# Kernel optimization log

Measured on AMD Instinct MI355X. Metric: run time of the kernel, lower is better.

## Reference

```python
import jax, jax.numpy as jnp
import numpy as np

N = 100_000      # nodes
E = 1_600_000    # directed edges (before self-loops)
F_IN = 256       # input node features
H = 128          # hidden_dim
HEADS = 2
C_HEAD = H // HEADS  # 64, GATConv out_channels per head
G = 128          # graphs in batch
NCLS = 10
NEG_SLOPE = 0.2  # PyG GATConv default


def setup_inputs() -> dict:
    key = jax.random.key(0)
    ks = jax.random.split(key, 20)
    p = lambda k, shape: (jax.random.normal(k, shape, jnp.float32) * 0.05)
    x = jax.random.normal(ks[0], (N, F_IN), jnp.float32)
    edge_index = jax.random.randint(ks[1], (2, E), 0, N, dtype=jnp.int64)
    batch = jnp.sort(jax.random.randint(ks[2], (N,), 0, G, dtype=jnp.int64))
    return dict(
        x=x, edge_index=edge_index, batch=batch,
        pre_w=p(ks[3], (F_IN, H)), pre_b=p(ks[4], (H,)),
        w1=p(ks[5], (H, H)), asrc1=p(ks[6], (HEADS, C_HEAD)), adst1=p(ks[7], (HEADS, C_HEAD)), b1=p(ks[8], (H,)),
        w2=p(ks[9], (H, H)), asrc2=p(ks[10], (HEADS, C_HEAD)), adst2=p(ks[11], (HEADS, C_HEAD)), b2=p(ks[12], (H,)),
        post_w1=p(ks[13], (H, H)), post_b1=p(ks[14], (H,)),
        post_w2=p(ks[15], (H, NCLS)), post_b2=p(ks[16], (NCLS,)),
    )


def _gat_conv(h_in, w, a_src, a_dst, b, src, dst):
    # h: [N, heads, c]
    h = (h_in @ w).reshape(N, HEADS, C_HEAD)
    alpha_src = jnp.sum(h * a_src, axis=-1)  # [N, heads]
    alpha_dst = jnp.sum(h * a_dst, axis=-1)  # [N, heads]
    e = jax.nn.leaky_relu(alpha_src[src] + alpha_dst[dst], NEG_SLOPE)  # [E+N, heads]
    # numerically stable softmax over incoming edges of each destination node
    m = jax.ops.segment_max(e, dst, num_segments=N)
    ex = jnp.exp(e - m[dst])
    denom = jax.ops.segment_sum(ex, dst, num_segments=N)
    alpha = ex / denom[dst]                                           # [E+N, heads]
    out = jax.ops.segment_sum(h[src] * alpha[:, :, None], dst, num_segments=N)
    return out.reshape(N, H) + b  # concat heads + bias


def reference(x, edge_index, batch, pre_w, pre_b,
              w1, asrc1, adst1, b1, w2, asrc2, adst2, b2,
              post_w1, post_b1, post_w2, post_b2):
    # PyG GATConv default add_self_loops=True
    loop = jnp.arange(N, dtype=edge_index.dtype)
    src = jnp.concatenate([edge_index[0], loop])
    dst = jnp.concatenate([edge_index[1], loop])

    h = jax.nn.relu(x @ pre_w + pre_b)
    reprs = jax.ops.segment_sum(h, batch, num_segments=G)
    h = jax.nn.relu(_gat_conv(h, w1, asrc1, adst1, b1, src, dst))
    reprs = reprs + jax.ops.segment_sum(h, batch, num_segments=G)
    h = jax.nn.relu(_gat_conv(h, w2, asrc2, adst2, b2, src, dst))
    reprs = reprs + jax.ops.segment_sum(h, batch, num_segments=G)
    z = jax.nn.relu(reprs @ post_w1 + post_b1) @ post_w2 + post_b2
    return jax.nn.log_softmax(z, axis=-1)
```

## Files before the change

### kernel.cpp

```cpp
#include <hip/hip_runtime.h>
#include <hip/hip_bf16.h>
#include <math.h>

#define NNODES 100000
#define NEDGES 1600000
#define FIN 256
#define HDIM 128
#define NGRAPH 128
#define NCLS 10
#define NEG 0.2f

#define NBUCK 98
#define EPB 4096
#define EBLK ((NEDGES + EPB - 1) / EPB)

typedef short bf8 __attribute__((ext_vector_type(8)));
typedef float f4 __attribute__((ext_vector_type(4)));
typedef float f2v __attribute__((ext_vector_type(2)));

__device__ __forceinline__ float lrelu(float x) { return x > 0.f ? x : NEG * x; }

__device__ __forceinline__ unsigned short f2bf(float f) {
  union { float f; unsigned int u; } v; v.f = f;
  unsigned int r = v.u + 0x7fffu + ((v.u >> 16) & 1u);
  return (unsigned short)(r >> 16);
}
__device__ __forceinline__ float bf2f(unsigned short u) {
  union { unsigned int u; float f; } v; v.u = ((unsigned int)u) << 16; return v.f;
}
__device__ __forceinline__ float fast_rcp(float x) {
  float r;
  asm("v_rcp_f32 %0, %1" : "=v"(r) : "v"(x));
  return r;
}
__device__ __forceinline__ unsigned cvt_pk_bf16(float lo, float hi) {
  unsigned r;
  asm("v_cvt_pk_bf16_f32 %0, %1, %2" : "=v"(r) : "v"(lo), "v"(hi));
  return r;
}
__device__ __forceinline__ unsigned short pk_fp8(float a, float b) {
  return (unsigned short)__builtin_amdgcn_cvt_pk_fp8_f32(a, b, 0, false);
}
__device__ __forceinline__ f2v pk_unpack_fp8(unsigned p) {
#if __has_builtin(__builtin_amdgcn_cvt_pk_f32_fp8)
  return __builtin_amdgcn_cvt_pk_f32_fp8((int)p, false);
#else
  f2v r;
  r.x = __builtin_amdgcn_cvt_f32_fp8(p, 0);
  r.y = __builtin_amdgcn_cvt_f32_fp8(p, 1);
  return r;
#endif
}

__global__ __launch_bounds__(256) void convert_transpose(const float* __restrict__ w,
                                                         unsigned short* __restrict__ wt,
                                                         int K) {
  int i = blockIdx.x * 256 + threadIdx.x;
  if (i >= K * 128) return;
  int k = i >> 7, n = i & 127;
  wt[n * K + k] = f2bf(w[(size_t)k * 128 + n]);
}

template<int K, int ABF16>
__global__ __launch_bounds__(256) void gemm_cstage(const void* __restrict__ Av,
                                                   const unsigned short* __restrict__ Bt,
                                                   const float* __restrict__ bias,
                                                   unsigned short* __restrict__ Cb,
                                                   unsigned short* __restrict__ Cp,
                                                   const float* __restrict__ a_src,
                                                   const float* __restrict__ a_dst,
                                                   float* __restrict__ o_as,
                                                   float* __restrict__ o_ad,
                                                   int M, int dorelu) {
  constexpr int NKT = K / 32;
  __shared__ alignas(16) char AL[NKT * 256 * 16];
  __shared__ alignas(16) char BL[4 * 512 * 16];
  int tid = threadIdx.x;
  int wv = tid >> 6, lane = tid & 63;
  int quad = lane >> 4, m16 = lane & 15;
  int row0 = blockIdx.x * 64;

  if (ABF16) {
    const unsigned short* A = (const unsigned short*)Av;
    constexpr int UPR = K / 8;
#pragma unroll
    for (int i = 0; i < (64 * UPR) / 256; ++i) {
      int m = i * 256 + tid;
      int row = m / UPR;
      int u = m & (UPR - 1);
      int rr = row0 + row; if (rr > M - 1) rr = M - 1;
      bf8 v = *(const bf8*)&A[(size_t)rr * K + u * 8];
      int kt = u >> 2, q = u & 3;
      int dst = (((kt * 256) + (row >> 4) * 64 + q * 16 + (row & 15)) * 16) ^ ((kt & 7) << 4);
      *(bf8*)(AL + dst) = v;
    }
  } else {
    const float* A = (const float*)Av;
    constexpr int UPRF = K / 4;
#pragma unroll
    for (int i = 0; i < (64 * UPRF) / 256; ++i) {
      int m = i * 256 + tid;
      int row = m / UPRF;
      int u = m & (UPRF - 1);
      int rr = row0 + row; if (rr > M - 1) rr = M - 1;
      float4 v = *(const float4*)&A[(size_t)rr * K + u * 4];
      int kt = u >> 3, q = (u >> 1) & 3;
      int dst = ((kt * 256 + (row >> 4) * 64 + q * 16 + (row & 15)) * 16 + (u & 1) * 8) ^ ((kt & 7) << 4);
      uint2 w; w.x = cvt_pk_bf16(v.x, v.y); w.y = cvt_pk_bf16(v.z, v.w);
      *(uint2*)(AL + dst) = w;
    }
  }

  auto stageB = [&](int ch) {
#pragma unroll
    for (int i = 0; i < 8; ++i) {
      int m = i * 256 + tid;
      int nrow = m >> 4;
      int u = m & 15;
      bf8 v = *(const bf8*)&Bt[(size_t)nrow * K + ch * 128 + u * 8];
      int ktl = u >> 2;
      int dst = ((ktl * 512 + (nrow >> 4) * 64 + (u & 3) * 16 + (nrow & 15)) * 16) ^ (ktl << 4);
      *(bf8*)(BL + dst) = v;
    }
  };

  f4 acc[8];
#pragma unroll
  for (int b = 0; b < 8; ++b) acc[b] = (f4){0.f, 0.f, 0.f, 0.f};

  stageB(0);
  __syncthreads();
  constexpr int NCH = K / 128;
#pragma unroll
  for (int ch = 0; ch < NCH; ++ch) {
    if (ch) { __syncthreads(); stageB(ch); __syncthreads(); }
#pragma unroll
    for (int ktl = 0; ktl < 4; ++ktl) {
      int kt = ch * 4 + ktl;
      bf8 af = *(const bf8*)(AL + ((((kt * 256) + wv * 64 + lane) * 16) ^ ((kt & 7) << 4)));
#pragma unroll
      for (int tn = 0; tn < 8; ++tn) {
        bf8 bm = *(const bf8*)(BL + (((ktl * 512 + tn * 64 + lane) * 16) ^ (ktl << 4)));
        acc[tn] = __builtin_amdgcn_mfma_f32_16x16x32_bf16(af, bm, acc[tn], 0, 0, 0);
      }
    }
  }

  if (Cp) {
    if (a_src) {
      float aS[8], aD[8];
#pragma unroll
      for (int tn = 0; tn < 4; ++tn) {
        aS[tn]     = a_src[tn * 16 + m16];
        aS[tn + 4] = a_src[64 + tn * 16 + m16];
        aD[tn]     = a_dst[tn * 16 + m16];
        aD[tn + 4] = a_dst[64 + tn * 16 + m16];
      }
#pragma unroll
      for (int r = 0; r < 4; ++r) {
        int row = row0 + wv * 16 + quad * 4 + r;
        float ps0 = 0.f, ps1 = 0.f, pd0 = 0.f, pd1 = 0.f;
#pragma unroll
        for (int tn = 0; tn < 4; ++tn) {
          float v0 = acc[tn][r], v1 = acc[tn + 4][r];
          ps0 = fmaf(v0, aS[tn], ps0);
          ps1 = fmaf(v1, aS[tn + 4], ps1);
          pd0 = fmaf(v0, aD[tn], pd0);
          pd1 = fmaf(v1, aD[tn + 4], pd1);
        }
#pragma unroll
        for (int o = 8; o; o >>= 1) {
          ps0 += __shfl_xor(ps0, o); ps1 += __shfl_xor(ps1, o);
          pd0 += __shfl_xor(pd0, o); pd1 += __shfl_xor(pd1, o);
        }
        if (m16 == 0 && row < M) {
          o_as[2 * row] = ps0; o_as[2 * row + 1] = ps1;
          o_ad[2 * row] = pd0; o_ad[2 * row + 1] = pd1;
        }
      }
    }
#pragma unroll
    for (int tn = 0; tn < 4; ++tn)
#pragma unroll
      for (int r = 0; r < 4; ++r) {
        int row = row0 + wv * 16 + quad * 4 + r;
        if (row < M) {
          Cp[(size_t)row * 64 + tn * 16 + m16] = pk_fp8(acc[tn][r], acc[tn + 4][r]);
        }
      }
  } else {
#pragma unroll
    for (int tn = 0; tn < 8; ++tn) {
      float bv = bias ? bias[tn * 16 + m16] : 0.f;
#pragma unroll
      for (int r = 0; r < 4; ++r) {
        int row = row0 + wv * 16 + quad * 4 + r;
        if (row < M) {
          float v = acc[tn][r] + bv;
          if (dorelu) v = fmaxf(v, 0.f);
          Cb[(size_t)row * 128 + tn * 16 + m16] = f2bf(v);
        }
      }
    }
  }
}

__global__ void find_starts(const int* __restrict__ batch, int* __restrict__ gstart) {
  int g = threadIdx.x;
  if (g > NGRAPH) return;
  if (g == NGRAPH) { gstart[g] = NNODES; return; }
  int lo = 0, hi = NNODES;
  while (lo < hi) { int mid = (lo + hi) >> 1; if (batch[mid] < g) lo = mid + 1; else hi = mid; }
  gstart[g] = lo;
}

__global__ __launch_bounds__(256) void bin_count(const int* __restrict__ edst,
                                                 int* __restrict__ blockHist) {
  __shared__ int hist[NBUCK];
  int t = threadIdx.x, blk = blockIdx.x;
  if (t < NBUCK) hist[t] = 0;
  __syncthreads();
  int e0 = blk * EPB;
#pragma unroll
  for (int it = 0; it < EPB / 256; ++it) {
    int e = e0 + it * 256 + t;
    if (e < NEDGES) atomicAdd(&hist[((unsigned)edst[e]) >> 10], 1);
  }
  __syncthreads();
  if (t < NBUCK) blockHist[blk * NBUCK + t] = hist[t];
}

__global__ __launch_bounds__(512) void colscan(const int* __restrict__ blockHist,
                                               int* __restrict__ blockBaseCol,
                                               int* __restrict__ bucket_total) {
  __shared__ int s[512];
  int b = blockIdx.x, t = threadIdx.x;
  int v = (t < EBLK) ? blockHist[t * NBUCK + b] : 0;
  s[t] = v;
  __syncthreads();
  for (int off = 1; off < 512; off <<= 1) {
    int u = (t >= off) ? s[t - off] : 0;
    __syncthreads();
    s[t] += u;
    __syncthreads();
  }
  if (t < EBLK) blockBaseCol[b * EBLK + t] = s[t] - v;
  if (t == 511) bucket_total[b] = s[511];
}

__global__ __launch_bounds__(128) void bscan(const int* __restrict__ bucket_total,
                                             int* __restrict__ bucket_ptr) {
  __shared__ int s[128];
  int t = threadIdx.x;
  int v = (t < NBUCK) ? bucket_total[t] : 0;
  s[t] = v;
  __syncthreads();
  for (int off = 1; off < 128; off <<= 1) {
    int u = (t >= off) ? s[t - off] : 0;
    __syncthreads();
    s[t] += u;
    __syncthreads();
  }
  if (t < NBUCK) bucket_ptr[t] = s[t] - v;
  if (t == 127) bucket_ptr[NBUCK] = s[127];
}

__global__ __launch_bounds__(512) void bin_place(const int* __restrict__ esrc,
                                                 const int* __restrict__ edst,
                                                 const int* __restrict__ blockBaseCol,
                                                 const int* __restrict__ bucket_ptr,
                                                 unsigned* __restrict__ stagingG) {
  __shared__ int hist[NBUCK + 1], lbase[NBUCK + 1], lcur[NBUCK + 1], cbase[NBUCK];
  __shared__ int tmp[128];
  __shared__ uint2 st[EPB];
  int t = threadIdx.x, blk = blockIdx.x;
  if (t < NBUCK + 1) hist[t] = 0;
  __syncthreads();
  int e0 = blk * EPB;
#pragma unroll
  for (int it = 0; it < EPB / 512; ++it) {
    int e = e0 + it * 512 + t;
    int b = NBUCK;
    if (e < NEDGES) b = ((unsigned)edst[e]) >> 10;
    atomicAdd(&hist[b], 1);
  }
  __syncthreads();
  if (t < 128) tmp[t] = (t < NBUCK + 1) ? hist[t] : 0;
  __syncthreads();
  for (int off = 1; off < 128; off <<= 1) {
    int u = 0;
    if (t < 128 && t >= off) u = tmp[t - off];
    __syncthreads();
    if (t < 128) tmp[t] += u;
    __syncthreads();
  }
  if (t < NBUCK + 1) { int ex = tmp[t] - hist[t]; lbase[t] = ex; lcur[t] = ex; }
  if (t < NBUCK) cbase[t] = bucket_ptr[t] + blockBaseCol[t * EBLK + blk];
  __syncthreads();
#pragma unroll
  for (int it = 0; it < EPB / 512; ++it) {
    int e = e0 + it * 512 + t;
    unsigned s = 0, d = 0xFFFFFFFFu;
    if (e < NEDGES) { s = (unsigned)esrc[e]; d = (unsigned)edst[e]; }
    int b = (d == 0xFFFFFFFFu) ? NBUCK : (int)(d >> 10);
    int slot = atomicAdd(&lcur[b], 1);
    st[slot] = make_uint2(s, d);
  }
  __syncthreads();
  for (int i = t; i < EPB; i += 512) {
    uint2 ed = st[i];
    if (ed.y == 0xFFFFFFFFu) continue;
    int b = (int)(ed.y >> 10);
    stagingG[cbase[b] + (i - lbase[b])] = ((ed.y & 1023u) << 17) | ed.x;
  }
}

__global__ __launch_bounds__(1024) void bucket_csr_fused(const unsigned* __restrict__ stagingG,
                                                         const int* __restrict__ bucket_ptr,
                                                         int* __restrict__ row_ptr,
                                                         int* __restrict__ colv) {
  __shared__ int dl[1024];
  __shared__ int cur[1024];
  int b = blockIdx.x, t = threadIdx.x;
  dl[t] = 0;
  __syncthreads();
  int s0 = bucket_ptr[b], s1 = bucket_ptr[b + 1];
  for (int j = s0 + t; j < s1; j += 1024)
    atomicAdd(&dl[stagingG[j] >> 17], 1);
  __syncthreads();
  int myDeg = dl[t];
  for (int off = 1; off < 1024; off <<= 1) {
    int u = (t >= off) ? dl[t - off] : 0;
    __syncthreads();
    dl[t] += u;
    __syncthreads();
  }
  int rp = s0 + dl[t] - myDeg;
  cur[t] = rp;
  int n = (b << 10) + t;
  if (n < NNODES) row_ptr[n] = rp;
  if (n == NNODES - 1) row_ptr[NNODES] = rp + myDeg;
  __syncthreads();
  for (int j = s0 + t; j < s1; j += 1024) {
    unsigned v = stagingG[j];
    int pos = atomicAdd(&cur[v >> 17], 1);
    colv[pos] = (int)(v & 0x1FFFFu);
  }
}

__global__ __launch_bounds__(256) void aggregate(const unsigned short* __restrict__ hwb,
                                                 const float* __restrict__ a_s,
                                                 const float* __restrict__ a_d,
                                                 const int* __restrict__ row_ptr,
                                                 const int* __restrict__ colv,
                                                 const float* __restrict__ bias,
                                                 unsigned short* __restrict__ out) {
  __shared__ float2 wsh[256];
  int i = (blockIdx.x * 256 + threadIdx.x) >> 6;
  int lane = threadIdx.x & 63;
  if (i >= NNODES) return;
  i = __builtin_amdgcn_readfirstlane(i);
  int wbase = (threadIdx.x >> 6) * 64;

  float ad0 = a_d[2 * i], ad1 = a_d[2 * i + 1];
  int start = row_ptr[i], end = row_ptr[i + 1];
  int deg = end - start;
  float ws0 = __expf(lrelu(a_s[2 * i] + ad0));
  float ws1 = __expf(lrelu(a_s[2 * i + 1] + ad1));

  int sl = 0; float w0l = 0.f, w1l = 0.f;
  if (lane < deg) {
    sl = colv[start + lane];
    float2 av = *reinterpret_cast<const float2*>(&a_s[2 * sl]);
    w0l = __expf(lrelu(av.x + ad0));
    w1l = __expf(lrelu(av.y + ad1));
  }
  wsh[wbase + lane] = make_float2(w0l, w1l);
  float d0 = w0l, d1 = w1l;
  for (int o = 32; o; o >>= 1) { d0 += __shfl_xor(d0, o); d1 += __shfl_xor(d1, o); }
  float den0 = d0 + ws0, den1 = d1 + ws1;

  unsigned ps = hwb[(size_t)i * 64 + lane];
  f2v pv = pk_unpack_fp8(ps);
  float acc0 = ws0 * pv.x, acc1 = ws1 * pv.y;

  int dmin = deg < 64 ? deg : 64;
  int t = 0;
#define GSTEP(T)                                                               \
  {                                                                            \
    int s = __builtin_amdgcn_readlane(sl, (T));                                \
    unsigned q = hwb[(size_t)s * 64 + lane];                                   \
    float2 w = wsh[wbase + (T)];                    \
    f2v xv = pk_unpack_fp8(q);                                                 \
    acc0 = fmaf(w.x, xv.x, acc0);                                              \
    acc1 = fmaf(w.y, xv.y, acc1);                                              \
  }
  for (; t + 8 <= dmin; t += 8) {
    GSTEP(t);     GSTEP(t + 1); GSTEP(t + 2); GSTEP(t + 3);
    GSTEP(t + 4); GSTEP(t + 5); GSTEP(t + 6); GSTEP(t + 7);
  }
  for (; t < dmin; ++t) { GSTEP(t); }
#undef GSTEP

  for (int j = start + 64; j < end; ++j) {
    int s = colv[j];
    float2 av = *reinterpret_cast<const float2*>(&a_s[2 * s]);
    float w0 = __expf(lrelu(av.x + ad0));
    float w1 = __expf(lrelu(av.y + ad1));
    den0 += w0; den1 += w1;
    unsigned q = hwb[(size_t)s * 64 + lane];
    f2v xv = pk_unpack_fp8(q);
    acc0 = fmaf(w0, xv.x, acc0);
    acc1 = fmaf(w1, xv.y, acc1);
  }

  float r0 = fast_rcp(den0), r1 = fast_rcp(den1);
  float o0 = fmaxf(acc0 * r0 + bias[lane], 0.f);
  float o1 = fmaxf(acc1 * r1 + bias[64 + lane], 0.f);
  unsigned pk = cvt_pk_bf16(o0, o1);
  out[(size_t)i * 128 + lane]      = (unsigned short)pk;
  out[(size_t)i * 128 + 64 + lane] = (unsigned short)(pk >> 16);
}

#define SEG_CHUNK 128
__global__ __launch_bounds__(128) void seg_sum_fast(const unsigned short* __restrict__ h,
                                                    const int* __restrict__ batch,
                                                    const int* __restrict__ gstart,
                                                    float* __restrict__ reprs) {
  int n0 = blockIdx.x * SEG_CHUNK;
  if (n0 >= NNODES) return;
  int nend = n0 + SEG_CHUNK; if (nend > NNODES) nend = NNODES;
  int tid = threadIdx.x;
  int r = n0;
  while (r < nend) {
    int g = batch[r];
    int segend = gstart[g + 1]; if (segend > nend) segend = nend;
    float a0 = 0.f, a1 = 0.f, a2 = 0.f, a3 = 0.f;
    for (; r + 3 < segend; r += 4) {
      a0 += bf2f(h[(size_t)r * 128 + tid]);
      a1 += bf2f(h[(size_t)(r + 1) * 128 + tid]);
      a2 += bf2f(h[(size_t)(r + 2) * 128 + tid]);
      a3 += bf2f(h[(size_t)(r + 3) * 128 + tid]);
    }
    for (; r < segend; ++r) a0 += bf2f(h[(size_t)r * 128 + tid]);
    atomicAdd(&reprs[g * 128 + tid], (a0 + a1) + (a2 + a3));
  }
}

__global__ __launch_bounds__(128) void head_kernel(const float* __restrict__ reprs,
                                                   const float* __restrict__ pw1,
                                                   const float* __restrict__ pb1,
                                                   const float* __restrict__ pw2,
                                                   const float* __restrict__ pb2,
                                                   float* __restrict__ out) {
  __shared__ float r[128], t1[128], z[NCLS];
  int g = blockIdx.x, tid = threadIdx.x;
  r[tid] = reprs[g * 128 + tid];
  __syncthreads();
  float acc = pb1[tid];
  for (int k = 0; k < 128; ++k) acc = fmaf(r[k], pw1[k * 128 + tid], acc);
  t1[tid] = fmaxf(acc, 0.f);
  __syncthreads();
  if (tid < NCLS) {
    float zz = pb2[tid];
    for (int k = 0; k < 128; ++k) zz = fmaf(t1[k], pw2[k * NCLS + tid], zz);
    z[tid] = zz;
  }
  __syncthreads();
  if (tid == 0) {
    float mx = -1e30f;
    for (int c = 0; c < NCLS; ++c) mx = fmaxf(mx, z[c]);
    float s = 0.f;
    for (int c = 0; c < NCLS; ++c) s += expf(z[c] - mx);
    float ls = logf(s) + mx;
    for (int c = 0; c < NCLS; ++c) out[g * NCLS + c] = z[c] - ls;
  }
}

extern "C" void kernel_launch(void* const* d_in, const int* in_sizes, int n_in,
                              void* d_out, int out_size, void* d_ws, size_t ws_size,
                              hipStream_t stream) {
  const float* x     = (const float*)d_in[0];
  const int*   eidx  = (const int*)d_in[1];
  const int*   batch = (const int*)d_in[2];
  const float* pre_w = (const float*)d_in[3];
  const float* pre_b = (const float*)d_in[4];
  const float* w1    = (const float*)d_in[5];
  const float* asrc1 = (const float*)d_in[6];
  const float* adst1 = (const float*)d_in[7];
  const float* b1    = (const float*)d_in[8];
  const float* w2    = (const float*)d_in[9];
  const float* asrc2 = (const float*)d_in[10];
  const float* adst2 = (const float*)d_in[11];
  const float* b2    = (const float*)d_in[12];
  const float* pw1   = (const float*)d_in[13];
  const float* pb1   = (const float*)d_in[14];
  const float* pw2   = (const float*)d_in[15];
  const float* pb2   = (const float*)d_in[16];
  float* out = (float*)d_out;

  const int* esrc = eidx;
  const int* edst = eidx + NEDGES;

  char* wsp = (char*)d_ws;
  size_t off = 0;
  auto alloc = [&](size_t bytes) -> void* {
    void* p = wsp + off;
    off += (bytes + 255) & ~(size_t)255;
    return p;
  };
  unsigned short* hb  = (unsigned short*)alloc((size_t)NNODES * 128 * 2);
  unsigned short* hwb = (unsigned short*)alloc((size_t)NNODES * 64 * 2);
  float* a_s         = (float*)alloc((size_t)NNODES * 2 * 4);
  float* a_d         = (float*)alloc((size_t)NNODES * 2 * 4);
  float* reprs       = (float*)alloc((size_t)NGRAPH * 128 * 4);
  int* gstart        = (int*)alloc((NGRAPH + 1) * 4);
  int* row_ptr       = (int*)alloc(((size_t)NNODES + 1) * 4);
  int* colv          = (int*)alloc((size_t)NEDGES * 4);
  unsigned short* wt_pre = (unsigned short*)alloc((size_t)128 * FIN * 2);
  unsigned short* wt1    = (unsigned short*)alloc((size_t)128 * HDIM * 2);
  unsigned short* wt2    = (unsigned short*)alloc((size_t)128 * HDIM * 2);
  int* blockHist     = (int*)alloc((size_t)EBLK * NBUCK * 4);
  int* blockBaseCol  = (int*)alloc((size_t)NBUCK * EBLK * 4);
  int* bucket_total  = (int*)alloc(NBUCK * 4);
  int* bucket_ptr    = (int*)alloc((NBUCK + 1) * 4);
  unsigned* stagingG = (unsigned*)alloc((size_t)NEDGES * 4);

  int wb = NNODES / 4;
  int sb = (NNODES + SEG_CHUNK - 1) / SEG_CHUNK;
  int gb = (NNODES + 63) / 64;

  convert_transpose<<<(FIN * 128 + 255) / 256, 256, 0, stream>>>(pre_w, wt_pre, FIN);
  convert_transpose<<<(HDIM * 128 + 255) / 256, 256, 0, stream>>>(w1, wt1, HDIM);
  convert_transpose<<<(HDIM * 128 + 255) / 256, 256, 0, stream>>>(w2, wt2, HDIM);

  hipMemsetAsync(reprs, 0, (size_t)NGRAPH * 128 * 4, stream);
  find_starts<<<1, 256, 0, stream>>>(batch, gstart);

  bin_count<<<EBLK, 256, 0, stream>>>(edst, blockHist);
  colscan<<<NBUCK, 512, 0, stream>>>(blockHist, blockBaseCol, bucket_total);
  bscan<<<1, 128, 0, stream>>>(bucket_total, bucket_ptr);
  bin_place<<<EBLK, 512, 0, stream>>>(esrc, edst, blockBaseCol, bucket_ptr, stagingG);
  bucket_csr_fused<<<NBUCK, 1024, 0, stream>>>(stagingG, bucket_ptr, row_ptr, colv);

  gemm_cstage<FIN, 0><<<gb, 256, 0, stream>>>(x, wt_pre, pre_b, hb, nullptr,
                                              nullptr, nullptr, nullptr, nullptr, NNODES, 1);
  seg_sum_fast<<<sb, 128, 0, stream>>>(hb, batch, gstart, reprs);

  gemm_cstage<HDIM, 1><<<gb, 256, 0, stream>>>(hb, wt1, nullptr, nullptr, hwb,
                                               asrc1, adst1, a_s, a_d, NNODES, 0);
  aggregate<<<wb, 256, 0, stream>>>(hwb, a_s, a_d, row_ptr, colv, b1, hb);
  seg_sum_fast<<<sb, 128, 0, stream>>>(hb, batch, gstart, reprs);

  gemm_cstage<HDIM, 1><<<gb, 256, 0, stream>>>(hb, wt2, nullptr, nullptr, hwb,
                                               asrc2, adst2, a_s, a_d, NNODES, 0);
  aggregate<<<wb, 256, 0, stream>>>(hwb, a_s, a_d, row_ptr, colv, b2, hb);
  seg_sum_fast<<<sb, 128, 0, stream>>>(hb, batch, gstart, reprs);

  head_kernel<<<NGRAPH, 128, 0, stream>>>(reprs, pw1, pb1, pw2, pb2, out);
}
```

Measured before the change: 470.3 us.

## Stream GEMM operands via global_load_lds with double-buffered K loop

Replaces the GEMM's full-A preload and chunked B staging with a double-buffered loop over 32-wide K slices. Each slice is loaded directly into LDS using global_load_lds 16-byte transfers, overlapping the next slice's load with the current MFMAs. For fp32 input, the bf16 conversion moves from staging to the LDS read. The per-wave loads are small (one 16-byte load per lane per slice) and there is a barrier every 32 K, which may limit how much of the load latency is hidden.

```diff
diff --git a/kernel.cpp b/kernel.cpp
--- a/kernel.cpp
+++ b/kernel.cpp
@@ -51,6 +51,11 @@
   return r;
 #endif
 }
+__device__ __forceinline__ void gload16(const void* gp, void* lp) {
+  __builtin_amdgcn_global_load_lds(
+      (const __attribute__((address_space(1))) void*)gp,
+      (__attribute__((address_space(3))) void*)lp, 16, 0, 0);
+}
 
 __global__ __launch_bounds__(256) void convert_transpose(const float* __restrict__ w,
                                                          unsigned short* __restrict__ wt,
@@ -62,88 +67,71 @@
 }
 
 template<int K, int ABF16>
-__global__ __launch_bounds__(256) void gemm_cstage(const void* __restrict__ Av,
-                                                   const unsigned short* __restrict__ Bt,
-                                                   const float* __restrict__ bias,
-                                                   unsigned short* __restrict__ Cb,
-                                                   unsigned short* __restrict__ Cp,
-                                                   const float* __restrict__ a_src,
-                                                   const float* __restrict__ a_dst,
-                                                   float* __restrict__ o_as,
-                                                   float* __restrict__ o_ad,
-                                                   int M, int dorelu) {
-  constexpr int NKT = K / 32;
-  __shared__ alignas(16) char AL[NKT * 256 * 16];
-  __shared__ alignas(16) char BL[4 * 512 * 16];
+__global__ __launch_bounds__(256) void gemm_gll(const void* __restrict__ Av,
+                                                const unsigned short* __restrict__ Bt,
+                                                const float* __restrict__ bias,
+                                                unsigned short* __restrict__ Cb,
+                                                unsigned short* __restrict__ Cp,
+                                                const float* __restrict__ a_src,
+                                                const float* __restrict__ a_dst,
+                                                float* __restrict__ o_as,
+                                                float* __restrict__ o_ad,
+                                                int M, int dorelu) {
+  constexpr int ABUF = ABF16 ? 4096 : 8192;
+  constexpr int SPAN = ABUF + 8192;
+  __shared__ alignas(16) char lds[2 * SPAN];
   int tid = threadIdx.x;
   int wv = tid >> 6, lane = tid & 63;
   int quad = lane >> 4, m16 = lane & 15;
   int row0 = blockIdx.x * 64;
-
-  if (ABF16) {
-    const unsigned short* A = (const unsigned short*)Av;
-    constexpr int UPR = K / 8;
-#pragma unroll
-    for (int i = 0; i < (64 * UPR) / 256; ++i) {
-      int m = i * 256 + tid;
-      int row = m / UPR;
-      int u = m & (UPR - 1);
-      int rr = row0 + row; if (rr > M - 1) rr = M - 1;
-      bf8 v = *(const bf8*)&A[(size_t)rr * K + u * 8];
-      int kt = u >> 2, q = u & 3;
-      int dst = (((kt * 256) + (row >> 4) * 64 + q * 16 + (row & 15)) * 16) ^ ((kt & 7) << 4);
-      *(bf8*)(AL + dst) = v;
+  int rA = row0 + wv * 16 + m16; if (rA > M - 1) rA = M - 1;
+  int nB0 = wv * 16 + m16, nB1 = (4 + wv) * 16 + m16;
+
+  const unsigned short* Ab = (const unsigned short*)Av;
+  const float* Af = (const float*)Av;
+
+  auto stage = [&](int buf, int kb) {
+    char* base = lds + buf * SPAN;
+    if (ABF16) {
+      gload16(&Ab[(size_t)rA * K + kb + quad * 8], base + wv * 1024);
+    } else {
+      gload16(&Af[(size_t)rA * K + kb + quad * 8],     base + wv * 2048);
+      gload16(&Af[(size_t)rA * K + kb + quad * 8 + 4], base + wv * 2048 + 1024);
     }
-  } else {
-    const float* A = (const float*)Av;
-    constexpr int UPRF = K / 4;
-#pragma unroll
-    for (int i = 0; i < (64 * UPRF) / 256; ++i) {
-      int m = i * 256 + tid;
-      int row = m / UPRF;
-      int u = m & (UPRF - 1);
-      int rr = row0 + row; if (rr > M - 1) rr = M - 1;
-      float4 v = *(const float4*)&A[(size_t)rr * K + u * 4];
-      int kt = u >> 3, q = (u >> 1) & 3;
-      int dst = ((kt * 256 + (row >> 4) * 64 + q * 16 + (row & 15)) * 16 + (u & 1) * 8) ^ ((kt & 7) << 4);
-      uint2 w; w.x = cvt_pk_bf16(v.x, v.y); w.y = cvt_pk_bf16(v.z, v.w);
-      *(uint2*)(AL + dst) = w;
+    char* bb = base + ABUF;
+    gload16(&Bt[(size_t)nB0 * K + kb + quad * 8], bb + wv * 1024);
+    gload16(&Bt[(size_t)nB1 * K + kb + quad * 8], bb + (4 + wv) * 1024);
+  };
+
+  f4 acc[8];
+#pragma unroll
+  for (int b = 0; b < 8; ++b) acc[b] = (f4){0.f, 0.f, 0.f, 0.f};
+
+  stage(0, 0);
+  int cur = 0;
+#pragma unroll
+  for (int kb = 0; kb < K; kb += 32) {
+    __syncthreads();
+    if (kb + 32 < K) stage(cur ^ 1, kb + 32);
+    const char* base = lds + cur * SPAN;
+    bf8 af;
+    if (ABF16) {
+      af = *(const bf8*)(base + wv * 1024 + lane * 16);
+    } else {
+      float4 x0 = *(const float4*)(base + wv * 2048 + lane * 16);
+      float4 x1 = *(const float4*)(base + wv * 2048 + 1024 + lane * 16);
+      union { bf8 v; unsigned u[4]; } r;
+      r.u[0] = cvt_pk_bf16(x0.x, x0.y); r.u[1] = cvt_pk_bf16(x0.z, x0.w);
+      r.u[2] = cvt_pk_bf16(x1.x, x1.y); r.u[3] = cvt_pk_bf16(x1.z, x1.w);
+      af = r.v;
     }
-  }
-
-  auto stageB = [&](int ch) {
-#pragma unroll
-    for (int i = 0; i < 8; ++i) {
-      int m = i * 256 + tid;
-      int nrow = m >> 4;
-      int u = m & 15;
-      bf8 v = *(const bf8*)&Bt[(size_t)nrow * K + ch * 128 + u * 8];
-      int ktl = u >> 2;
-      int dst = ((ktl * 512 + (nrow >> 4) * 64 + (u & 3) * 16 + (nrow & 15)) * 16) ^ (ktl << 4);
-      *(bf8*)(BL + dst) = v;
+    const char* bb = base + ABUF;
+#pragma unroll
+    for (int tn = 0; tn < 8; ++tn) {
+      bf8 bm = *(const bf8*)(bb + tn * 1024 + lane * 16);
+      acc[tn] = __builtin_amdgcn_mfma_f32_16x16x32_bf16(af, bm, acc[tn], 0, 0, 0);
     }
-  };
-
-  f4 acc[8];
-#pragma unroll
-  for (int b = 0; b < 8; ++b) acc[b] = (f4){0.f, 0.f, 0.f, 0.f};
-
-  stageB(0);
-  __syncthreads();
-  constexpr int NCH = K / 128;
-#pragma unroll
-  for (int ch = 0; ch < NCH; ++ch) {
-    if (ch) { __syncthreads(); stageB(ch); __syncthreads(); }
-#pragma unroll
-    for (int ktl = 0; ktl < 4; ++ktl) {
-      int kt = ch * 4 + ktl;
-      bf8 af = *(const bf8*)(AL + ((((kt * 256) + wv * 64 + lane) * 16) ^ ((kt & 7) << 4)));
-#pragma unroll
-      for (int tn = 0; tn < 8; ++tn) {
-        bf8 bm = *(const bf8*)(BL + (((ktl * 512 + tn * 64 + lane) * 16) ^ (ktl << 4)));
-        acc[tn] = __builtin_amdgcn_mfma_f32_16x16x32_bf16(af, bm, acc[tn], 0, 0, 0);
-      }
-    }
+    cur ^= 1;
   }
 
   if (Cp) {
@@ -543,17 +531,17 @@
   bin_place<<<EBLK, 512, 0, stream>>>(esrc, edst, blockBaseCol, bucket_ptr, stagingG);
   bucket_csr_fused<<<NBUCK, 1024, 0, stream>>>(stagingG, bucket_ptr, row_ptr, colv);
 
-  gemm_cstage<FIN, 0><<<gb, 256, 0, stream>>>(x, wt_pre, pre_b, hb, nullptr,
-                                              nullptr, nullptr, nullptr, nullptr, NNODES, 1);
+  gemm_gll<FIN, 0><<<gb, 256, 0, stream>>>(x, wt_pre, pre_b, hb, nullptr,
+                                           nullptr, nullptr, nullptr, nullptr, NNODES, 1);
   seg_sum_fast<<<sb, 128, 0, stream>>>(hb, batch, gstart, reprs);
 
-  gemm_cstage<HDIM, 1><<<gb, 256, 0, stream>>>(hb, wt1, nullptr, nullptr, hwb,
-                                               asrc1, adst1, a_s, a_d, NNODES, 0);
+  gemm_gll<HDIM, 1><<<gb, 256, 0, stream>>>(hb, wt1, nullptr, nullptr, hwb,
+                                            asrc1, adst1, a_s, a_d, NNODES, 0);
   aggregate<<<wb, 256, 0, stream>>>(hwb, a_s, a_d, row_ptr, colv, b1, hb);
   seg_sum_fast<<<sb, 128, 0, stream>>>(hb, batch, gstart, reprs);
 
-  gemm_cstage<HDIM, 1><<<gb, 256, 0, stream>>>(hb, wt2, nullptr, nullptr, hwb,
-                                               asrc2, adst2, a_s, a_d, NNODES, 0);
+  gemm_gll<HDIM, 1><<<gb, 256, 0, stream>>>(hb, wt2, nullptr, nullptr, hwb,
+                                            asrc2, adst2, a_s, a_d, NNODES, 0);
   aggregate<<<wb, 256, 0, stream>>>(hwb, a_s, a_d, row_ptr, colv, b2, hb);
   seg_sum_fast<<<sb, 128, 0, stream>>>(hb, batch, gstart, reprs);
 
```

Result: no change. 467.8 us (-0.5%).
